# Kernel optimization log

Measured on AMD Instinct MI355X. Metric: run time of the kernel, lower is better.

The kernel has to match this reference:

```python
import jax, jax.numpy as jnp
import numpy as np

ALPHA, BETA, GAMMA = 0.05, 0.95, 0.95
GDEP = 2
HID = 64
IN_DIM = 3
OUT_DIM = 3
OUT_LEN = 12
PPH = 12.0  # points_per_hour
INV_SQRT2 = 0.7071067811865476


def _rownorm(a):
    # preprocessing(): add self-loop, row-normalize
    a = a + jnp.eye(a.shape[0], dtype=a.dtype)
    return a / jnp.sum(a, axis=-1, keepdims=True)


def _gcrn(x, A, P, W, b):
    # DGCRN-style diffusion conv: h <- a*x + b*A h + g*P h, concat hops, mlp
    h = x
    out = [x]
    for _ in range(GDEP):
        h = (ALPHA * x
             + BETA * jnp.einsum('bvc,vw->bwc', h, A)
             + GAMMA * jnp.einsum('bvc,vw->bwc', h, P))
        out.append(h)
    return jnp.concatenate(out, -1) @ W + b


def _cell_step(xin, H, A1, A1T, P, W, b):
    # one GRU-style step; W/b stacked as [gz1, gz2, gr1, gr2, gc1, gc2]
    comb = jnp.concatenate([xin, H], -1)
    z = jax.nn.sigmoid(_gcrn(comb, A1, P, W[0], b[0]) + _gcrn(comb, A1T, P, W[1], b[1]))
    r = jax.nn.sigmoid(_gcrn(comb, A1, P, W[2], b[2]) + _gcrn(comb, A1T, P, W[3], b[3]))
    temp = jnp.concatenate([xin, r * H], -1)
    C = jnp.tanh(_gcrn(temp, A1, P, W[4], b[4]) + _gcrn(temp, A1T, P, W[5], b[5]))
    H = z * H + (1.0 - z) * C
    return H, C


def _encode(xs, H0, C0, A1, A1T, P, W, b):
    def body(carry, xin):
        H, C = _cell_step(xin, carry[0], A1, A1T, P, W, b)
        return (H, C), None
    (H, C), _ = jax.lax.scan(body, (H0, C0), xs)
    return H, C


def _forward(x, seqs_time, adj, predefined_A, H1_0, C1_0, H2_0, C2_0,
             W_encD, b_encD, W_encAD, b_encAD, W_dec, b_dec, W_fc, b_fc,
             W_aggH, b_aggH, W_aggC, b_aggC, W_camH, b_camH, W_camC, b_camC,
             wL, bL, wH, bH):
    B, Cin, N, T = x.shape
    A1 = _rownorm(adj)
    A1T = _rownorm(adj.T)
    P = predefined_A
    # level-1 db1 (Haar) wavelet along time
    xe, xo = x[..., 0::2], x[..., 1::2]
    xAD = (xe + xo) * INV_SQRT2  # approximation coeffs (B,C,N,T/2)
    xD = (xe - xo) * INV_SQRT2   # detail coeffs
    # downsampled time-of-day index feature
    hour = (seqs_time[:, -2, :] + 0.5) * 23.0
    minute = (seqs_time[:, -1, :] + 0.5) * 59.0
    hidx = jnp.floor((hour * 60.0 + minute) / (60.0 / PPH))  # (B,T)
    t_ds = hidx[:, ::2]                                      # (B,T/2)
    Th = xD.shape[-1]
    tfeat = jnp.broadcast_to(t_ds.T[:, :, None, None], (Th, B, N, 1)).astype(x.dtype)
    xsD = jnp.concatenate([jnp.transpose(xD, (3, 0, 2, 1)), tfeat], -1)   # (Th,B,N,in+1)
    xsAD = jnp.concatenate([jnp.transpose(xAD, (3, 0, 2, 1)), tfeat], -1)
    H1, C1 = _encode(xsD, H1_0, C1_0, A1, A1T, P, W_encD, b_encD)
    H2, C2 = _encode(xsAD, H2_0, C2_0, A1, A1T, P, W_encAD, b_encAD)
    # learnable IDWT fusion + interleave (even cols = L, odd cols = H)
    def fuse(a, b2):
        L = (a * wL + bL) + (b2 * wL + bL)
        Hh = (a * wH + bH) + (b2 * wH + bH)
        return jnp.stack([L, Hh], -1).reshape(B, N, 2 * HID)
    Hm, Cm = fuse(H1, H2), fuse(C1, C2)
    # out_dim=3 <= 6 -> 0.3*cam + 0.7*agg branch
    H = 0.3 * (Hm @ W_camH + b_camH) + 0.7 * (jnp.concatenate([H1, H2], -1) @ W_aggH + b_aggH)
    C = 0.3 * (Cm @ W_camC + b_camC) + 0.7 * (jnp.concatenate([C1, C2], -1) @ W_aggC + b_aggC)
    # decoder (eval path, no curriculum sampling)
    tod = jnp.floor((seqs_time[:, 2, :] + 0.5) * 6.0)  # (B,T)
    todf = jnp.broadcast_to(tod.T[:OUT_LEN, :, None, None], (OUT_LEN, B, N, 1)).astype(x.dtype)
    def dec_body(carry, t):
        Hc, Cc, din = carry
        xin = jnp.concatenate([din, t], -1)  # (B,N,out_dim+1)
        Hc, Cc = _cell_step(xin, Hc, A1, A1T, P, W_dec, b_dec)
        out = Hc @ W_fc + b_fc               # (B,N,out_dim)
        return (Hc, Cc, out), out
    _, ys = jax.lax.scan(dec_body, (H, C, jnp.zeros((B, N, OUT_DIM), x.dtype)), todf)
    # replicate torch stack(dim=1).view(B,N,out_dim,out_len).permute(0,2,1,3)
    flat = jnp.transpose(ys, (1, 2, 0, 3)).reshape(B, N, OUT_DIM, OUT_LEN)
    return jnp.transpose(flat, (0, 2, 1, 3))


def setup_inputs() -> dict:
    key = jax.random.key(0)
    ks = jax.random.split(key, 24)
    B, N, T = 32, 325, 12
    d = {}
    d['x'] = jax.random.normal(ks[0], (B, IN_DIM, N, T), jnp.float32)
    d['seqs_time'] = jax.random.uniform(ks[1], (B, 4, T), jnp.float32) - 0.5
    d['adj'] = jax.random.uniform(ks[2], (N, N), jnp.float32)
    Pa = jax.random.uniform(ks[3], (N, N), jnp.float32)
    d['predefined_A'] = Pa / jnp.sum(Pa, -1, keepdims=True)
    for i, nm in enumerate(['H1_0', 'C1_0', 'H2_0', 'C2_0']):
        d[nm] = jax.random.normal(ks[4 + i], (B, N, HID), jnp.float32) * 0.1
    dim_in = (GDEP + 1) * (IN_DIM + HID + 1)  # 204
    for i, nm in enumerate(['W_encD', 'W_encAD', 'W_dec']):
        d[nm] = jax.random.normal(ks[8 + i], (6, dim_in, HID), jnp.float32) * 0.02
        d['b' + nm[1:]] = jnp.zeros((6, HID), jnp.float32)
    d['W_fc'] = jax.random.normal(ks[11], (HID, OUT_DIM), jnp.float32) * 0.02
    d['b_fc'] = jnp.zeros((OUT_DIM,), jnp.float32)
    for i, nm in enumerate(['aggH', 'aggC', 'camH', 'camC']):
        d['W_' + nm] = jax.random.normal(ks[12 + i], (2 * HID, HID), jnp.float32) * 0.02
        d['b_' + nm] = jnp.zeros((HID,), jnp.float32)
    d['wL'] = jax.random.normal(ks[16], (N, HID), jnp.float32) * 0.1
    d['bL'] = jnp.zeros((N, HID), jnp.float32)
    d['wH'] = jax.random.normal(ks[17], (N, HID), jnp.float32) * 0.1
    d['bH'] = jnp.zeros((N, HID), jnp.float32)
    return d


def reference(x, seqs_time, adj, predefined_A, H1_0, C1_0, H2_0, C2_0,
              W_encD, b_encD, W_encAD, b_encAD, W_dec, b_dec, W_fc, b_fc,
              W_aggH, b_aggH, W_aggC, b_aggC, W_camH, b_camH, W_camC, b_camC,
              wL, bL, wH, bH):
    return _forward(x, seqs_time, adj, predefined_A, H1_0, C1_0, H2_0, C2_0,
                    W_encD, b_encD, W_encAD, b_encAD, W_dec, b_dec, W_fc, b_fc,
                    W_aggH, b_aggH, W_aggC, b_aggC, W_camH, b_camH, W_camC, b_camC,
                    wL, bL, wH, bH)
```

## Files before the change

kernel.cpp:

```cpp
#include <hip/hip_runtime.h>
#include <math.h>

#define NN 325
#define BB 32
#define NB (NN*BB)
#define TENC 6
#define TDEC 12
#define WSET 65472
#define WT_SET (192*352)
#define M_SET (325*192)
#define G16_MAT (384*352)
#define PT_B 765952ull
#define PT_E 1531904ull
#define DP_B 3660800ull
#define DP_E 7321600ull

typedef _Float16 f16;
typedef f16 f16x4 __attribute__((ext_vector_type(4)));
typedef f16 f16x8 __attribute__((ext_vector_type(8)));
typedef float f32x4 __attribute__((ext_vector_type(4)));

static constexpr float ALPHA = 0.05f;
static constexpr float BETA  = 0.95f;
static constexpr float GAMMA = 0.95f;
static constexpr float ISQ2  = 0.7071067811865476f;

static constexpr size_t OFF_G    = 0;
static constexpr size_t OFF_RS   = OFF_G + 2ull*NN*NN;
static constexpr size_t OFF_RV   = OFF_RS + 650;
static constexpr size_t OFF_WEFF = OFF_RV + 1300;
static constexpr size_t OFF_WT   = OFF_WEFF + 3ull*WSET;
static constexpr size_t OFF_G16  = OFF_WT + (3ull*WT_SET)/2;
static constexpr size_t OFF_M    = OFF_G16 + (4ull*G16_MAT)/2;
static constexpr size_t OFF_WF   = OFF_M + 3ull*M_SET;
static constexpr size_t OFF_TV   = OFF_WF + 8192;
static constexpr size_t OFF_XS   = OFF_TV + 576;
static constexpr size_t OFF_PT   = OFF_XS + (2ull*TENC*NB*4)/2;
static constexpr size_t OFF_DP   = OFF_PT + (2ull*PT_E)/2;
static constexpr size_t OFF_ZR   = OFF_DP + (2ull*DP_E)/2;
static constexpr size_t OFF_HENC = OFF_ZR + 2ull*NB*64;
static constexpr size_t OFF_HDEC = OFF_HENC + 2ull*NB*64;

__device__ inline unsigned pk2(float a, float b) {
    union { f16 h[2]; unsigned u; } x;
    x.h[0] = (f16)a; x.h[1] = (f16)b; return x.u;
}
__device__ inline void st4h(f16* p, float a, float b, float c, float d) {
    f16x4 v; v[0]=(f16)a; v[1]=(f16)b; v[2]=(f16)c; v[3]=(f16)d;
    *(f16x4*)p = v;
}
__device__ inline f16x8 ld8_lds(const f16* p) {
    f16x4 lo = *(const f16x4*)p;
    f16x4 hi = *(const f16x4*)(p + 4);
    f16x8 r;
    r[0]=lo[0]; r[1]=lo[1]; r[2]=lo[2]; r[3]=lo[3];
    r[4]=hi[0]; r[5]=hi[1]; r[6]=hi[2]; r[7]=hi[3];
    return r;
}

__global__ void k_sums(const float* __restrict__ adj, float* rs, float* cs) {
    int v = blockIdx.x; int t = threadIdx.x;
    float sr = 0.f, sc = 0.f;
    for (int w = t; w < NN; w += 64) { sr += adj[v*NN + w]; sc += adj[w*NN + v]; }
    for (int o = 32; o > 0; o >>= 1) { sr += __shfl_down(sr, o); sc += __shfl_down(sc, o); }
    if (t == 0) { rs[v] = sr + 1.0f; cs[v] = sc + 1.0f; }
}

__global__ void k_buildG(const float* __restrict__ adj, const float* __restrict__ P,
                         const float* __restrict__ rs, const float* __restrict__ cs,
                         float* __restrict__ G) {
    int idx = blockIdx.x*256 + threadIdx.x;
    if (idx >= NN*NN) return;
    int w = idx / NN, v = idx % NN;
    float d = (v == w) ? 1.0f : 0.0f;
    float a1  = (adj[v*NN + w] + d) / rs[v];
    float a1t = (adj[w*NN + v] + d) / cs[v];
    float p = P[v*NN + w];
    G[idx]         = BETA*a1  + GAMMA*p;
    G[NN*NN + idx] = BETA*a1t + GAMMA*p;
}

__global__ __launch_bounds__(256) void k_gg(const float* __restrict__ G, float* __restrict__ G2) {
    int g = blockIdx.z;
    const float* A = G + (size_t)g*NN*NN;
    float* C = G2 + (size_t)g*NN*NN;
    int n0 = blockIdx.y*32, j0 = blockIdx.x*32;
    int tx = threadIdx.x & 31, ty = threadIdx.x >> 5;
    __shared__ float As[32][33];
    __shared__ float Bs[32][33];
    float acc[4] = {};
    for (int k0 = 0; k0 < NN; k0 += 32) {
        for (int l = threadIdx.x; l < 32*32; l += 256) {
            int i = l >> 5, kk = l & 31;
            int n = n0 + i, k = k0 + kk;
            As[i][kk] = (n < NN && k < NN) ? A[(size_t)n*NN + k] : 0.0f;
            int j = j0 + kk;
            Bs[i][kk] = (k0 + i < NN && j < NN) ? A[(size_t)(k0+i)*NN + j] : 0.0f;
        }
        __syncthreads();
        #pragma unroll 8
        for (int kk = 0; kk < 32; kk++) {
            float bv = Bs[kk][tx];
            #pragma unroll
            for (int i = 0; i < 4; i++) acc[i] = fmaf(As[ty + 8*i][kk], bv, acc[i]);
        }
        __syncthreads();
    }
    #pragma unroll
    for (int i = 0; i < 4; i++) {
        int n = n0 + ty + 8*i, j = j0 + tx;
        if (n < NN && j < NN) C[(size_t)n*NN + j] = acc[i];
    }
}

__global__ void k_g16(const float* __restrict__ G, const float* __restrict__ G2,
                      f16* __restrict__ G16) {
    int idx = blockIdx.x*256 + threadIdx.x;
    if (idx >= 4*G16_MAT) return;
    int m = idx / G16_MAT;
    int rem = idx - m*G16_MAT;
    int n = rem / 352, v = rem - n*352;
    int g = m >> 1, s = m & 1;
    float val = 0.0f;
    if (n < NN && v < NN) {
        float gv = G[(size_t)g*NN*NN + n*NN + v];
        float d = (n == v) ? ALPHA : 0.0f;
        val = (s == 0) ? (gv + d)
                       : (G2[(size_t)g*NN*NN + n*NN + v] + ALPHA*gv + d);
    }
    G16[idx] = (f16)val;
}

__global__ void k_rowsum(const float* __restrict__ G, const float* __restrict__ G2,
                         float* __restrict__ rv) {
    int row = blockIdx.x;
    int g = row / NN, n = row - g*NN;
    int t = threadIdx.x;
    float s1 = 0.f, s2 = 0.f;
    for (int v = t; v < NN; v += 64) {
        s1 += G[(size_t)g*NN*NN + n*NN + v];
        s2 += G2[(size_t)g*NN*NN + n*NN + v];
    }
    for (int o = 32; o > 0; o >>= 1) { s1 += __shfl_down(s1, o); s2 += __shfl_down(s2, o); }
    if (t == 0) {
        rv[(g*2 + 0)*NN + n] = ALPHA + s1;
        rv[(g*2 + 1)*NN + n] = ALPHA + ALPHA*s1 + s2;
    }
}

__global__ void k_weff3(const float* __restrict__ W0, const float* __restrict__ b0,
                        const float* __restrict__ W1, const float* __restrict__ b1,
                        const float* __restrict__ W2, const float* __restrict__ b2,
                        float* __restrict__ WeffAll) {
    int s = blockIdx.y;
    const float* W = (s == 0) ? W0 : (s == 1) ? W1 : W2;
    const float* b = (s == 0) ? b0 : (s == 1) ? b1 : b2;
    float* Wset = WeffAll + (size_t)s*WSET;
    float* Wzr = Wset;
    float* Wc  = Wset + 43520;
    float* bzr = Wset + 65280;
    float* bc  = Wset + 65408;
    int tid = blockIdx.x*256 + threadIdx.x;
    if (tid < 340*192) {
        int k = tid / 192, col = tid % 192;
        int g = col >> 6, oo = col & 63;
        const float* Wa = W + (2*g)*204*64;
        const float* Wb = W + (2*g+1)*204*64;
        float val;
        if (k < 68)       val = Wa[k*64+oo] + Wb[k*64+oo];
        else if (k < 204) val = Wa[k*64+oo];
        else              val = Wb[(k-136)*64+oo];
        if (g < 2) Wzr[k*128 + g*64 + oo] = val;
        else       Wc[k*64 + oo] = val;
    }
    if (blockIdx.x == 0 && threadIdx.x < 192) {
        int col = threadIdx.x, g = col >> 6, oo = col & 63;
        float bv = b[(2*g)*64+oo] + b[(2*g+1)*64+oo];
        if (g < 2) bzr[col] = bv; else bc[oo] = bv;
    }
}

__global__ void k_wt3(const float* __restrict__ WeffAll, f16* __restrict__ WtAll) {
    int s = blockIdx.y;
    const float* Weff = WeffAll + (size_t)s*WSET;
    f16* Wt = WtAll + (size_t)s*WT_SET;
    int idx = blockIdx.x*256 + threadIdx.x;
    if (idx >= 192*352) return;
    int o = idx / 352, k = idx - o*352;
    float v = 0.0f;
    if (k < 340) {
        int p = k / 68, c = k - p*68;
        if (c != 3) v = (o < 128) ? Weff[k*128 + o] : Weff[43520 + k*64 + (o - 128)];
    }
    Wt[idx] = (f16)v;
}

__global__ void k_M3(const float* __restrict__ WeffAll, const float* __restrict__ rv,
                     float* __restrict__ MAll) {
    int s = blockIdx.y;
    const float* Weff = WeffAll + (size_t)s*WSET;
    float* M = MAll + (size_t)s*M_SET;
    int idx = blockIdx.x*256 + threadIdx.x;
    if (idx >= 325*192) return;
    int n = idx / 192, q = idx - n*192;
    float acc;
    if (q < 128) {
        int o = q;
        acc = Weff[3*128 + o];
        #pragma unroll
        for (int p = 1; p <= 4; p++)
            acc += rv[(p-1)*NN + n] * Weff[(p*68 + 3)*128 + o];
        M[(size_t)n*128 + o] = acc;
    } else {
        int o = q - 128;
        acc = Weff[43520 + 3*64 + o];
        #pragma unroll
        for (int p = 1; p <= 4; p++)
            acc += rv[(p-1)*NN + n] * Weff[43520 + (p*68 + 3)*64 + o];
        M[325*128 + (size_t)n*64 + o] = acc;
    }
}

__global__ void k_wfuse(const float* __restrict__ Wcam, const float* __restrict__ Wagg,
                        f16* __restrict__ Wf) {
    int idx = blockIdx.x*256 + threadIdx.x;
    if (idx >= 64*256) return;
    int o = idx >> 8, k = idx & 255;
    float v = (k < 128) ? 0.3f*Wcam[(size_t)k*64 + o]
                        : 0.7f*Wagg[(size_t)(k-128)*64 + o];
    Wf[(size_t)o*256 + k] = (f16)v;
}

__global__ void k_tv(const float* __restrict__ st, float* __restrict__ tv) {
    int idx = blockIdx.x*256 + threadIdx.x;
    if (idx >= 18*32) return;
    int b = idx & 31, t = idx >> 5;
    float v;
    if (t < 6) {
        float hour   = (st[b*48 + 24 + 2*t] + 0.5f) * 23.0f;
        float minute = (st[b*48 + 36 + 2*t] + 0.5f) * 59.0f;
        v = floorf((hour*60.0f + minute) / 5.0f);
    } else {
        int td = t - 6;
        v = floorf((st[b*48 + 24 + td] + 0.5f) * 6.0f);
    }
    tv[idx] = v;
}

__global__ void k_xs16(const float* __restrict__ x, f16* __restrict__ xs) {
    int idx = blockIdx.x*256 + threadIdx.x;
    if (idx >= 2*TENC*NB*4) return;
    int c = idx & 3;
    int r = (idx >> 2) % NB;
    int t = (idx / (4*NB)) % TENC;
    int e = idx / (4*NB*TENC);
    int n = r / BB, b = r % BB;
    float val = 0.0f;
    if (c < 3) {
        float xe = x[((b*3 + c)*NN + n)*12 + 2*t];
        float xo = x[((b*3 + c)*NN + n)*12 + 2*t + 1];
        val = (e == 0) ? (xe - xo)*ISQ2 : (xe + xo)*ISQ2;
    }
    xs[idx] = (f16)val;
}

__global__ void k_initH(const float* __restrict__ H1_0, const float* __restrict__ H2_0,
                        float* __restrict__ Henc) {
    int idx = blockIdx.x*256 + threadIdx.x;
    if (idx >= 2*NB*64) return;
    int k = idx & 63;
    int r = (idx >> 6) % NB;
    int e = idx / (NB*64);
    int n = r / BB, b = r % BB;
    const float* src = e ? H2_0 : H1_0;
    Henc[idx] = src[((size_t)b*NN + n)*64 + k];
}

__global__ void k_initDP(const f16* __restrict__ xs, const float* __restrict__ H1_0,
                         const float* __restrict__ H2_0, f16* __restrict__ DP) {
    int idx = blockIdx.x*256 + threadIdx.x;
    if (idx >= 2*NB*92) return;
    int cc = idx % 92;
    int r = (idx / 92) % NB;
    int e = idx / (92*NB);
    int n = r >> 5, b = r & 31;
    f16* D0 = DP + (size_t)e*DP_E;
    if (cc < 68) {
        f16 v;
        if (cc < 3)       v = xs[(size_t)e*TENC*NB*4 + (size_t)r*4 + cc];
        else if (cc == 3) v = (f16)0.0f;
        else {
            const float* h0 = e ? H2_0 : H1_0;
            v = (f16)h0[((size_t)b*NN + n)*64 + (cc-4)];
        }
        D0[(size_t)r*352 + cc] = v;
    } else if (cc < 80) {
        D0[(size_t)r*352 + 340 + (cc-68)] = (f16)0.0f;
    } else {
        D0[DP_B + (size_t)r*352 + 340 + (cc-80)] = (f16)0.0f;
    }
}

__global__ void k_initPT(const f16* __restrict__ xs, const float* __restrict__ H1_0,
                         const float* __restrict__ H2_0, f16* __restrict__ PTb) {
    int idx = blockIdx.x*256 + threadIdx.x;
    if (idx >= 2*2176*352) return;
    int v = idx % 352;
    int j = (idx / 352) % 2176;
    int e = idx / (352*2176);
    f16* P0 = PTb + (size_t)e*PT_E;
    if (v >= NN) {
        P0[(size_t)j*352 + v] = (f16)0.0f;
        P0[PT_B + (size_t)j*352 + v] = (f16)0.0f;
        return;
    }
    int b = j / 68, c = j - b*68;
    f16 val;
    if (c < 3)       val = xs[(size_t)e*TENC*NB*4 + (size_t)(v*32+b)*4 + c];
    else if (c == 3) val = (f16)0.0f;
    else {
        const float* h0 = e ? H2_0 : H1_0;
        val = (f16)h0[((size_t)b*NN + v)*64 + (c-4)];
    }
    P0[(size_t)j*352 + v] = val;
}

struct KParams {
    const f16* G16;
    f16* PT;
    f16* DP;
    const f16* Wt;
    const float* Weff;
    const float* Mw;
    const float* tv;
    float* ZR;
    float* Henc;
    float* Hdec;
    const f16* xs;
    const float* wL; const float* bL; const float* wH; const float* bH;
    const float* bcam; const float* bagg;
    const f16* Wfuse;
    const float* Wfc; const float* bfc;
    float* out;
};

__device__ void phase_diff(const KParams& p, int par, int E) {
    int tid = threadIdx.x;
    int lane = tid & 63, w = tid >> 6;
    int wm = w >> 1, wn = w & 1;
    int l15 = lane & 15, lk = lane >> 4;
    int ntiles = 34*21*E;
    for (int idx = blockIdx.x; idx < ntiles; idx += gridDim.x) {
        int jt = idx % 34, rem = idx / 34;
        int Rt = rem % 21, e = rem / 21;
        const f16* X = p.PT + (size_t)e*PT_E + (size_t)par*PT_B;
        f16* D = p.DP + (size_t)e*DP_E + (size_t)par*DP_B;
        int j0 = jt*64, R0 = Rt*64;
        const f16* ap[2];
        #pragma unroll
        for (int a = 0; a < 2; a++)
            ap[a] = X + (size_t)(j0 + wm*32 + a*16 + l15)*352;
        const f16* bp[2]; int mv[2], nv[2];
        #pragma unroll
        for (int bt = 0; bt < 2; bt++) {
            int R = R0 + wn*32 + bt*16 + l15;
            int ok = (R < 1300);
            int Rc = ok ? R : 0;
            int m = Rc / 325, n = Rc - m*325;
            mv[bt] = ok ? m : -1; nv[bt] = n;
            bp[bt] = p.G16 + (size_t)m*G16_MAT + (size_t)n*352;
        }
        f32x4 acc[2][2] = {};
        #pragma unroll
        for (int k0 = 0; k0 < 352; k0 += 32) {
            f16x8 af[2], bf[2];
            #pragma unroll
            for (int a = 0; a < 2; a++) af[a] = *(const f16x8*)(ap[a] + k0 + lk*8);
            #pragma unroll
            for (int bt = 0; bt < 2; bt++) bf[bt] = *(const f16x8*)(bp[bt] + k0 + lk*8);
            #pragma unroll
            for (int a = 0; a < 2; a++)
                #pragma unroll
                for (int bt = 0; bt < 2; bt++)
                    acc[a][bt] = __builtin_amdgcn_mfma_f32_16x16x32_f16(af[a], bf[bt], acc[a][bt], 0,0,0);
        }
        #pragma unroll
        for (int bt = 0; bt < 2; bt++) {
            if (mv[bt] < 0) continue;
            int m = mv[bt], n = nv[bt];
            #pragma unroll
            for (int a = 0; a < 2; a++) {
                int jb = j0 + wm*32 + a*16 + lk*4;
                int b = jb / 68, c = jb - b*68;
                f16* dst = D + (size_t)(n*32 + b)*352 + (m+1)*68 + c;
                st4h(dst, acc[a][bt][0], acc[a][bt][1], acc[a][bt][2], acc[a][bt][3]);
            }
        }
    }
}

__device__ void phase_proj0(const KParams& p, int par, int E,
        const f16* WtB, int wt_str, const float* biasB, int bias_str,
        const float* MB, int m_str, const float* tvp, float* HstB) {
    int tid = threadIdx.x;
    int lane = tid & 63, w = tid >> 6;
    int wm = w >> 1, wn = w & 1;
    int l15 = lane & 15, lk = lane >> 4;
    int ntiles = 2*163*E;
    for (int idx = blockIdx.x; idx < ntiles; idx += gridDim.x) {
        int ob = idx & 1, rem = idx >> 1;
        int rt = rem % 163, e = rem / 163;
        const f16* Wt = WtB + (size_t)e*wt_str;
        const float* bias = biasB + (size_t)e*bias_str + 65280;
        const float* M = MB + (size_t)e*m_str;
        const f16* Dc = p.DP + (size_t)e*DP_E + (size_t)par*DP_B;
        f16* Dn = p.DP + (size_t)e*DP_E + (size_t)(par^1)*DP_B;
        f16* PTn = p.PT + (size_t)e*PT_E + (size_t)(par^1)*PT_B;
        float* ZR = p.ZR + (size_t)e*NB*64;
        float* Hs = HstB + (size_t)e*NB*64;
        int o0 = ob*64, r0 = rt*64;
        const f16* ap[2]; const f16* bp[2];
        #pragma unroll
        for (int a = 0; a < 2; a++) ap[a] = Wt + (size_t)(o0 + wm*32 + a*16 + l15)*352;
        #pragma unroll
        for (int bt = 0; bt < 2; bt++) bp[bt] = Dc + (size_t)(r0 + wn*32 + bt*16 + l15)*352;
        f32x4 acc[2][2] = {};
        #pragma unroll
        for (int k0 = 0; k0 < 352; k0 += 32) {
            f16x8 af[2], bf[2];
            #pragma unroll
            for (int a = 0; a < 2; a++) af[a] = *(const f16x8*)(ap[a] + k0 + lk*8);
            #pragma unroll
            for (int bt = 0; bt < 2; bt++) bf[bt] = *(const f16x8*)(bp[bt] + k0 + lk*8);
            #pragma unroll
            for (int a = 0; a < 2; a++)
                #pragma unroll
                for (int bt = 0; bt < 2; bt++)
                    acc[a][bt] = __builtin_amdgcn_mfma_f32_16x16x32_f16(af[a], bf[bt], acc[a][bt], 0,0,0);
        }
        #pragma unroll
        for (int bt = 0; bt < 2; bt++) {
            int r = r0 + wn*32 + bt*16 + l15;
            if (r < NB) {
                int n = r >> 5, b = r & 31;
                float tvb = tvp[b];
                #pragma unroll
                for (int a = 0; a < 2; a++) {
                    int oo = o0 + wm*32 + a*16 + lk*4;
                    float4 bs = *(const float4*)(bias + oo);
                    float4 ms = *(const float4*)(M + (size_t)n*128 + oo);
                    float p0 = acc[a][bt][0] + bs.x + tvb*ms.x;
                    float p1 = acc[a][bt][1] + bs.y + tvb*ms.y;
                    float p2 = acc[a][bt][2] + bs.z + tvb*ms.z;
                    float p3 = acc[a][bt][3] + bs.w + tvb*ms.w;
                    float s0 = 1.0f/(1.0f+expf(-p0)), s1 = 1.0f/(1.0f+expf(-p1));
                    float s2 = 1.0f/(1.0f+expf(-p2)), s3 = 1.0f/(1.0f+expf(-p3));
                    if (oo < 64) {
                        *(float4*)(ZR + (size_t)r*64 + oo) = make_float4(s0,s1,s2,s3);
                    } else {
                        int oh = oo - 64;
                        float4 h4 = *(const float4*)(Hs + (size_t)r*64 + oh);
                        float g0 = s0*h4.x, g1 = s1*h4.y, g2 = s2*h4.z, g3 = s3*h4.w;
                        st4h(Dn + (size_t)r*352 + 4 + oh, g0, g1, g2, g3);
                        size_t pb = (size_t)(b*68 + 4 + oh)*352 + n;
                        PTn[pb]       = (f16)g0;
                        PTn[pb + 352] = (f16)g1;
                        PTn[pb + 704] = (f16)g2;
                        PTn[pb + 1056]= (f16)g3;
                    }
                }
            }
        }
        if (ob == 0) {
            int row = tid >> 2, q = tid & 3;
            int r = r0 + row;
            if (r < NB) {
                f16 v = Dc[(size_t)r*352 + q];
                Dn[(size_t)r*352 + q] = v;
                PTn[(size_t)((r & 31)*68 + q)*352 + (r >> 5)] = v;
            }
        }
    }
}

__device__ void phase_proj1_enc(const KParams& p, int par, int t) {
    int tid = threadIdx.x;
    int lane = tid & 63, w = tid >> 6;
    int wm = w >> 1, wn = w & 1;
    int l15 = lane & 15, lk = lane >> 4;
    int ntiles = 163*2;
    for (int idx = blockIdx.x; idx < ntiles; idx += gridDim.x) {
        int rt = idx % 163, e = idx / 163;
        const f16* Wt = p.Wt + (size_t)e*WT_SET + 128*352;
        const float* bias = p.Weff + (size_t)e*WSET + 65408;
        const float* M = p.Mw + (size_t)e*M_SET + 325*128;
        const f16* Dc = p.DP + (size_t)e*DP_E + (size_t)par*DP_B;
        f16* Dn = p.DP + (size_t)e*DP_E + (size_t)(par^1)*DP_B;
        f16* PTn = p.PT + (size_t)e*PT_E + (size_t)(par^1)*PT_B;
        float* ZR = p.ZR + (size_t)e*NB*64;
        float* Hs = p.Henc + (size_t)e*NB*64;
        const float* tvv = p.tv + (size_t)t*32;
        int r0 = rt*64;
        const f16* ap[2]; const f16* bp[2];
        #pragma unroll
        for (int a = 0; a < 2; a++) ap[a] = Wt + (size_t)(wm*32 + a*16 + l15)*352;
        #pragma unroll
        for (int bt = 0; bt < 2; bt++) bp[bt] = Dc + (size_t)(r0 + wn*32 + bt*16 + l15)*352;
        f32x4 acc[2][2] = {};
        #pragma unroll
        for (int k0 = 0; k0 < 352; k0 += 32) {
            f16x8 af[2], bf[2];
            #pragma unroll
            for (int a = 0; a < 2; a++) af[a] = *(const f16x8*)(ap[a] + k0 + lk*8);
            #pragma unroll
            for (int bt = 0; bt < 2; bt++) bf[bt] = *(const f16x8*)(bp[bt] + k0 + lk*8);
            #pragma unroll
            for (int a = 0; a < 2; a++)
                #pragma unroll
                for (int bt = 0; bt < 2; bt++)
                    acc[a][bt] = __builtin_amdgcn_mfma_f32_16x16x32_f16(af[a], bf[bt], acc[a][bt], 0,0,0);
        }
        #pragma unroll
        for (int bt = 0; bt < 2; bt++) {
            int r = r0 + wn*32 + bt*16 + l15;
            if (r < NB) {
                int n = r >> 5, b = r & 31;
                float tvb = tvv[b];
                #pragma unroll
                for (int a = 0; a < 2; a++) {
                    int oo = wm*32 + a*16 + lk*4;
                    float4 bs = *(const float4*)(bias + oo);
                    float4 ms = *(const float4*)(M + (size_t)n*64 + oo);
                    float p0 = acc[a][bt][0] + bs.x + tvb*ms.x;
                    float p1 = acc[a][bt][1] + bs.y + tvb*ms.y;
                    float p2 = acc[a][bt][2] + bs.z + tvb*ms.z;
                    float p3 = acc[a][bt][3] + bs.w + tvb*ms.w;
                    float4 z4 = *(const float4*)(ZR + (size_t)r*64 + oo);
                    float4 h4 = *(const float4*)(Hs + (size_t)r*64 + oo);
                    float h0 = z4.x*h4.x + (1.0f - z4.x)*tanhf(p0);
                    float h1 = z4.y*h4.y + (1.0f - z4.y)*tanhf(p1);
                    float h2 = z4.z*h4.z + (1.0f - z4.z)*tanhf(p2);
                    float h3 = z4.w*h4.w + (1.0f - z4.w)*tanhf(p3);
                    *(float4*)(Hs + (size_t)r*64 + oo) = make_float4(h0,h1,h2,h3);
                    st4h(Dn + (size_t)r*352 + 4 + oo, h0, h1, h2, h3);
                    size_t pb = (size_t)(b*68 + 4 + oo)*352 + n;
                    PTn[pb]       = (f16)h0;
                    PTn[pb + 352] = (f16)h1;
                    PTn[pb + 704] = (f16)h2;
                    PTn[pb + 1056]= (f16)h3;
                }
            }
        }
        const f16* xn = nullptr;
        if (t < TENC-1) xn = p.xs + (size_t)(e*TENC + t + 1)*NB*4;
        if (xn) {
            int row = tid >> 2, q = tid & 3;
            int r = r0 + row;
            if (r < NB) {
                f16 v = (q < 3) ? xn[(size_t)r*4 + q] : (f16)0.0f;
                Dn[(size_t)r*352 + q] = v;
                PTn[(size_t)((r & 31)*68 + q)*352 + (r >> 5)] = v;
            }
        }
    }
}

__device__ void phase_proj1_dec(const KParams& p, int par, int t, f16* smem) {
    int tid = threadIdx.x;
    int lane = tid & 63, w = tid >> 6;
    int wm = w >> 1, wn = w & 1;
    int l15 = lane & 15, lk = lane >> 4;
    const f16* Wt = p.Wt + 2*WT_SET + 128*352;
    const float* bias = p.Weff + 2*WSET + 65408;
    const float* M = p.Mw + 2*M_SET + 325*128;
    const f16* Dc = p.DP + (size_t)par*DP_B;
    f16* Dn = p.DP + (size_t)(par^1)*DP_B;
    f16* PTn = p.PT + (size_t)(par^1)*PT_B;
    const float* tvv = p.tv + (size_t)(6 + t)*32;
    for (int idx = blockIdx.x; idx < 163; idx += gridDim.x) {
        int r0 = idx*64;
        const f16* ap[2]; const f16* bp[2];
        #pragma unroll
        for (int a = 0; a < 2; a++) ap[a] = Wt + (size_t)(wm*32 + a*16 + l15)*352;
        #pragma unroll
        for (int bt = 0; bt < 2; bt++) bp[bt] = Dc + (size_t)(r0 + wn*32 + bt*16 + l15)*352;
        f32x4 acc[2][2] = {};
        #pragma unroll
        for (int k0 = 0; k0 < 352; k0 += 32) {
            f16x8 af[2], bf[2];
            #pragma unroll
            for (int a = 0; a < 2; a++) af[a] = *(const f16x8*)(ap[a] + k0 + lk*8);
            #pragma unroll
            for (int bt = 0; bt < 2; bt++) bf[bt] = *(const f16x8*)(bp[bt] + k0 + lk*8);
            #pragma unroll
            for (int a = 0; a < 2; a++)
                #pragma unroll
                for (int bt = 0; bt < 2; bt++)
                    acc[a][bt] = __builtin_amdgcn_mfma_f32_16x16x32_f16(af[a], bf[bt], acc[a][bt], 0,0,0);
        }
        #pragma unroll
        for (int bt = 0; bt < 2; bt++) {
            int r = r0 + wn*32 + bt*16 + l15;
            int rl = wn*32 + bt*16 + l15;
            if (r < NB) {
                int n = r >> 5, b = r & 31;
                float tvb = tvv[b];
                #pragma unroll
                for (int a = 0; a < 2; a++) {
                    int oo = wm*32 + a*16 + lk*4;
                    float4 bs = *(const float4*)(bias + oo);
                    float4 ms = *(const float4*)(M + (size_t)n*64 + oo);
                    float p0 = acc[a][bt][0] + bs.x + tvb*ms.x;
                    float p1 = acc[a][bt][1] + bs.y + tvb*ms.y;
                    float p2 = acc[a][bt][2] + bs.z + tvb*ms.z;
                    float p3 = acc[a][bt][3] + bs.w + tvb*ms.w;
                    float4 z4 = *(const float4*)(p.ZR + (size_t)r*64 + oo);
                    float4 h4 = *(const float4*)(p.Hdec + (size_t)r*64 + oo);
                    float h0 = z4.x*h4.x + (1.0f - z4.x)*tanhf(p0);
                    float h1 = z4.y*h4.y + (1.0f - z4.y)*tanhf(p1);
                    float h2 = z4.z*h4.z + (1.0f - z4.z)*tanhf(p2);
                    float h3 = z4.w*h4.w + (1.0f - z4.w)*tanhf(p3);
                    *(float4*)(p.Hdec + (size_t)r*64 + oo) = make_float4(h0,h1,h2,h3);
                    st4h(Dn + (size_t)r*352 + 4 + oo, h0, h1, h2, h3);
                    size_t pb = (size_t)(b*68 + 4 + oo)*352 + n;
                    PTn[pb]       = (f16)h0;
                    PTn[pb + 352] = (f16)h1;
                    PTn[pb + 704] = (f16)h2;
                    PTn[pb + 1056]= (f16)h3;
                    st4h(smem + rl*68 + oo, h0, h1, h2, h3);
                }
            }
        }
        __syncthreads();
        for (int q = tid; q < 192; q += 256) {
            int row = q / 3, c = q - row*3;
            int r = r0 + row;
            if (r < NB) {
                float a = p.bfc[c];
                #pragma unroll 8
                for (int k = 0; k < 64; k++)
                    a = fmaf((float)smem[row*68 + k], p.Wfc[k*3 + c], a);
                int n = r >> 5, b = r & 31;
                int qq = t*3 + c;
                int oq = qq / 12, lq = qq - oq*12;
                p.out[(((size_t)b*3 + oq)*NN + n)*12 + lq] = a;
                if (t < TDEC-1) {
                    Dn[(size_t)r*352 + c] = (f16)a;
                    PTn[(size_t)((r & 31)*68 + c)*352 + (r >> 5)] = (f16)a;
                }
            }
        }
        if (t < TDEC-1 && tid < 64) {
            int r = r0 + tid;
            if (r < NB) {
                Dn[(size_t)r*352 + 3] = (f16)0.0f;
                PTn[(size_t)((r & 31)*68 + 3)*352 + (r >> 5)] = (f16)0.0f;
            }
        }
        __syncthreads();
    }
}

__device__ void phase_fuse(const KParams& p, f16* smem) {
    int tid = threadIdx.x;
    int lane = tid & 63, wave = tid >> 6;
    int wm = wave >> 1, wn = wave & 1;
    int l15 = lane & 15, lk = lane >> 4;
    const float* H1 = p.Henc;
    const float* H2 = p.Henc + (size_t)NB*64;
    unsigned* La = (unsigned*)smem;
    f16* Dn = p.DP;
    f16* PTn = p.PT;
    for (int idx = blockIdx.x; idx < 163; idx += gridDim.x) {
        int r0 = idx*64;
        for (int l = tid; l < 64*64; l += 256) {
            int i = l >> 6, k = l & 63;
            int r = r0 + i;
            unsigned val = 0;
            if (r < NB) {
                int n = r >> 5;
                float h1 = H1[(size_t)r*64 + k], h2 = H2[(size_t)r*64 + k];
                float s = h1 + h2;
                val = pk2(s*p.wL[n*64+k] + 2.0f*p.bL[n*64+k],
                          s*p.wH[n*64+k] + 2.0f*p.bH[n*64+k]);
            }
            La[i*132 + k] = val;
        }
        for (int l = tid; l < 64*32; l += 256) {
            int i = l >> 5, kp = l & 31;
            int r = r0 + i;
            unsigned v1 = 0, v2 = 0;
            if (r < NB) {
                float2 a = *(const float2*)(H1 + (size_t)r*64 + 2*kp);
                float2 b = *(const float2*)(H2 + (size_t)r*64 + 2*kp);
                v1 = pk2(a.x, a.y);
                v2 = pk2(b.x, b.y);
            }
            La[i*132 + 64 + kp] = v1;
            La[i*132 + 96 + kp] = v2;
        }
        __syncthreads();
        f32x4 acc[2][2] = {};
        for (int k0 = 0; k0 < 256; k0 += 32) {
            f16x8 afr[2], bfr[2];
            #pragma unroll
            for (int a = 0; a < 2; a++)
                afr[a] = ld8_lds(smem + (wm*32 + a*16 + l15)*264 + k0 + lk*8);
            #pragma unroll
            for (int b = 0; b < 2; b++)
                bfr[b] = *(const f16x8*)(p.Wfuse + (size_t)(wn*32 + b*16 + l15)*256 + k0 + lk*8);
            #pragma unroll
            for (int a = 0; a < 2; a++)
                #pragma unroll
                for (int b = 0; b < 2; b++)
                    acc[a][b] = __builtin_amdgcn_mfma_f32_16x16x32_f16(afr[a], bfr[b], acc[a][b], 0,0,0);
        }
        #pragma unroll
        for (int a = 0; a < 2; a++) {
            #pragma unroll
            for (int b = 0; b < 2; b++) {
                int o = wn*32 + b*16 + l15;
                float bo = 0.3f*p.bcam[o] + 0.7f*p.bagg[o];
                #pragma unroll
                for (int rr = 0; rr < 4; rr++) {
                    int r = r0 + wm*32 + a*16 + lk*4 + rr;
                    if (r >= NB) continue;
                    float val = acc[a][b][rr] + bo;
                    p.Hdec[(size_t)r*64 + o] = val;
                    Dn[(size_t)r*352 + 4 + o] = (f16)val;
                    PTn[(size_t)((r & 31)*68 + 4 + o)*352 + (r >> 5)] = (f16)val;
                }
            }
        }
        {
            int r = r0 + (tid >> 2), q = tid & 3;
            if (r < NB) {
                Dn[(size_t)r*352 + q] = (f16)0.0f;
                PTn[(size_t)((r & 31)*68 + q)*352 + (r >> 5)] = (f16)0.0f;
            }
        }
        __syncthreads();
    }
}

__global__ __launch_bounds__(256) void g_diff(KParams p, int par, int E) { phase_diff(p, par, E); }
__global__ __launch_bounds__(256) void g_proj0e(KParams p, int par, int t) {
    phase_proj0(p, par, 2, p.Wt, WT_SET, p.Weff, WSET, p.Mw, M_SET,
                p.tv + (size_t)t*32, p.Henc);
}
__global__ __launch_bounds__(256) void g_proj0d(KParams p, int par, int t) {
    phase_proj0(p, par, 1, p.Wt + 2*WT_SET, 0, p.Weff + 2*WSET, 0,
                p.Mw + 2*M_SET, 0, p.tv + (size_t)(6 + t)*32, p.Hdec);
}
__global__ __launch_bounds__(256) void g_proj1e(KParams p, int par, int t) { phase_proj1_enc(p, par, t); }
__global__ __launch_bounds__(256) void g_proj1d(KParams p, int par, int t) {
    __shared__ f16 smem[64*68];
    phase_proj1_dec(p, par, t, smem);
}
__global__ __launch_bounds__(256) void g_fuse(KParams p) {
    __shared__ f16 smem[64*264];
    phase_fuse(p, smem);
}

extern "C" void kernel_launch(void* const* d_in, const int* in_sizes, int n_in,
                              void* d_out, int out_size, void* d_ws, size_t ws_size,
                              hipStream_t stream) {
    const float* x      = (const float*)d_in[0];
    const float* st     = (const float*)d_in[1];
    const float* adj    = (const float*)d_in[2];
    const float* P      = (const float*)d_in[3];
    const float* H1_0   = (const float*)d_in[4];
    const float* H2_0   = (const float*)d_in[6];
    const float* W_encD = (const float*)d_in[8];
    const float* b_encD = (const float*)d_in[9];
    const float* W_encAD= (const float*)d_in[10];
    const float* b_encAD= (const float*)d_in[11];
    const float* W_dec  = (const float*)d_in[12];
    const float* b_dec  = (const float*)d_in[13];
    const float* W_fc   = (const float*)d_in[14];
    const float* b_fc   = (const float*)d_in[15];
    const float* W_aggH = (const float*)d_in[16];
    const float* b_aggH = (const float*)d_in[17];
    const float* W_camH = (const float*)d_in[20];
    const float* b_camH = (const float*)d_in[21];
    const float* wL     = (const float*)d_in[24];
    const float* bL     = (const float*)d_in[25];
    const float* wH     = (const float*)d_in[26];
    const float* bH     = (const float*)d_in[27];

    float* ws   = (float*)d_ws;
    float* G    = ws + OFF_G;
    float* rs   = ws + OFF_RS;
    float* cs   = rs + NN;
    float* rv   = ws + OFF_RV;
    float* Weff = ws + OFF_WEFF;
    f16*   Wt   = (f16*)(ws + OFF_WT);
    f16*   G16  = (f16*)(ws + OFF_G16);
    float* Mw   = ws + OFF_M;
    f16*   Wf   = (f16*)(ws + OFF_WF);
    float* tv   = ws + OFF_TV;
    f16*   xs   = (f16*)(ws + OFF_XS);
    f16*   PT   = (f16*)(ws + OFF_PT);
    f16*   DP   = (f16*)(ws + OFF_DP);
    float* ZR   = ws + OFF_ZR;
    float* G2   = ZR;
    float* Henc = ws + OFF_HENC;
    float* Hdec = ws + OFF_HDEC;

    k_sums<<<NN, 64, 0, stream>>>(adj, rs, cs);
    k_buildG<<<(NN*NN + 255)/256, 256, 0, stream>>>(adj, P, rs, cs, G);
    k_gg<<<dim3(11,11,2), 256, 0, stream>>>(G, G2);
    k_g16<<<(4*G16_MAT + 255)/256, 256, 0, stream>>>(G, G2, G16);
    k_rowsum<<<650, 64, 0, stream>>>(G, G2, rv);
    k_weff3<<<dim3(255,3), 256, 0, stream>>>(W_encD, b_encD, W_encAD, b_encAD,
                                             W_dec, b_dec, Weff);
    k_wt3<<<dim3((192*352 + 255)/256, 3), 256, 0, stream>>>(Weff, Wt);
    k_M3<<<dim3((325*192 + 255)/256, 3), 256, 0, stream>>>(Weff, rv, Mw);
    k_wfuse<<<64, 256, 0, stream>>>(W_camH, W_aggH, Wf);
    k_tv<<<3, 256, 0, stream>>>(st, tv);
    k_xs16<<<(2*TENC*NB*4 + 255)/256, 256, 0, stream>>>(x, xs);
    k_initH<<<(2*NB*64 + 255)/256, 256, 0, stream>>>(H1_0, H2_0, Henc);
    k_initDP<<<(2*NB*92 + 255)/256, 256, 0, stream>>>(xs, H1_0, H2_0, DP);
    k_initPT<<<(2*2176*352 + 255)/256, 256, 0, stream>>>(xs, H1_0, H2_0, PT);

    KParams prm;
    prm.G16 = G16; prm.PT = PT; prm.DP = DP;
    prm.Wt = Wt; prm.Weff = Weff; prm.Mw = Mw; prm.tv = tv;
    prm.ZR = ZR; prm.Henc = Henc; prm.Hdec = Hdec;
    prm.xs = xs;
    prm.wL = wL; prm.bL = bL; prm.wH = wH; prm.bH = bH;
    prm.bcam = b_camH; prm.bagg = b_aggH; prm.Wfuse = Wf;
    prm.Wfc = W_fc; prm.bfc = b_fc;
    prm.out = (float*)d_out;

    int par = 0;
    for (int t = 0; t < TENC; t++) {
        g_diff<<<1428, 256, 0, stream>>>(prm, par, 2);
        g_proj0e<<<652, 256, 0, stream>>>(prm, par, t);
        par ^= 1;
        g_diff<<<1428, 256, 0, stream>>>(prm, par, 2);
        g_proj1e<<<326, 256, 0, stream>>>(prm, par, t);
        par ^= 1;
    }
    g_fuse<<<163, 256, 0, stream>>>(prm);
    for (int t = 0; t < TDEC; t++) {
        g_diff<<<714, 256, 0, stream>>>(prm, par, 1);
        g_proj0d<<<326, 256, 0, stream>>>(prm, par, t);
        par ^= 1;
        g_diff<<<714, 256, 0, stream>>>(prm, par, 1);
        g_proj1d<<<163, 256, 0, stream>>>(prm, par, t);
        par ^= 1;
    }
}
```

Before: 1.358 ms.

## Remap projection row tiles to node-major groups for coalesced transposed writes

Projection and fuse kernels now tile rows as 32 consecutive nodes times 2 batch columns, replacing 64 consecutive flattened rows. The transposed PT buffer is indexed by node along its contiguous dimension, so each tile's scattered f16 stores become runs of adjacent nodes. The cost is extra padded tiles (176 instead of 163, with idle lanes in the last node group) and strided reads of the D rows. The fuse kernel also swaps MFMA operand roles so its outputs can be written as float4 and 4-wide f16 stores.

```diff
diff --git a/kernel.cpp b/kernel.cpp
--- a/kernel.cpp
+++ b/kernel.cpp
@@ -14,6 +14,7 @@
 #define PT_E 1531904ull
 #define DP_B 3660800ull
 #define DP_E 7321600ull
+#define NGB 176
 
 typedef _Float16 f16;
 typedef f16 f16x4 __attribute__((ext_vector_type(4)));
@@ -406,10 +407,11 @@
     int lane = tid & 63, w = tid >> 6;
     int wm = w >> 1, wn = w & 1;
     int l15 = lane & 15, lk = lane >> 4;
-    int ntiles = 2*163*E;
+    int ntiles = 2*NGB*E;
     for (int idx = blockIdx.x; idx < ntiles; idx += gridDim.x) {
         int ob = idx & 1, rem = idx >> 1;
-        int rt = rem % 163, e = rem / 163;
+        int rt = rem % NGB, e = rem / NGB;
+        int ng = rt >> 4, bpx = rt & 15;
         const f16* Wt = WtB + (size_t)e*wt_str;
         const float* bias = biasB + (size_t)e*bias_str + 65280;
         const float* M = MB + (size_t)e*m_str;
@@ -418,12 +420,18 @@
         f16* PTn = p.PT + (size_t)e*PT_E + (size_t)(par^1)*PT_B;
         float* ZR = p.ZR + (size_t)e*NB*64;
         float* Hs = HstB + (size_t)e*NB*64;
-        int o0 = ob*64, r0 = rt*64;
-        const f16* ap[2]; const f16* bp[2];
+        int o0 = ob*64;
+        int bcol = bpx*2 + wn;
+        const f16* ap[2]; const f16* bfp[2];
         #pragma unroll
         for (int a = 0; a < 2; a++) ap[a] = Wt + (size_t)(o0 + wm*32 + a*16 + l15)*352;
         #pragma unroll
-        for (int bt = 0; bt < 2; bt++) bp[bt] = Dc + (size_t)(r0 + wn*32 + bt*16 + l15)*352;
+        for (int bt = 0; bt < 2; bt++) {
+            int n = ng*32 + bt*16 + l15;
+            int r = n*32 + bcol;
+            int rc = (n < NN) ? r : 0;
+            bfp[bt] = Dc + (size_t)rc*352;
+        }
         f32x4 acc[2][2] = {};
         #pragma unroll
         for (int k0 = 0; k0 < 352; k0 += 32) {
@@ -431,7 +439,7 @@
             #pragma unroll
             for (int a = 0; a < 2; a++) af[a] = *(const f16x8*)(ap[a] + k0 + lk*8);
             #pragma unroll
-            for (int bt = 0; bt < 2; bt++) bf[bt] = *(const f16x8*)(bp[bt] + k0 + lk*8);
+            for (int bt = 0; bt < 2; bt++) bf[bt] = *(const f16x8*)(bfp[bt] + k0 + lk*8);
             #pragma unroll
             for (int a = 0; a < 2; a++)
                 #pragma unroll
@@ -440,9 +448,10 @@
         }
         #pragma unroll
         for (int bt = 0; bt < 2; bt++) {
-            int r = r0 + wn*32 + bt*16 + l15;
-            if (r < NB) {
-                int n = r >> 5, b = r & 31;
+            int n = ng*32 + bt*16 + l15;
+            if (n < NN) {
+                int b = bcol;
+                int r = n*32 + b;
                 float tvb = tvp[b];
                 #pragma unroll
                 for (int a = 0; a < 2; a++) {
@@ -472,12 +481,14 @@
             }
         }
         if (ob == 0) {
-            int row = tid >> 2, q = tid & 3;
-            int r = r0 + row;
-            if (r < NB) {
+            int n_l = tid & 31, b_l = (tid >> 5) & 1, q = tid >> 6;
+            int n = ng*32 + n_l;
+            if (n < NN) {
+                int b = bpx*2 + b_l;
+                int r = n*32 + b;
                 f16 v = Dc[(size_t)r*352 + q];
                 Dn[(size_t)r*352 + q] = v;
-                PTn[(size_t)((r & 31)*68 + q)*352 + (r >> 5)] = v;
+                PTn[(size_t)(b*68 + q)*352 + n] = v;
             }
         }
     }
@@ -488,9 +499,10 @@
     int lane = tid & 63, w = tid >> 6;
     int wm = w >> 1, wn = w & 1;
     int l15 = lane & 15, lk = lane >> 4;
-    int ntiles = 163*2;
+    int ntiles = NGB*2;
     for (int idx = blockIdx.x; idx < ntiles; idx += gridDim.x) {
-        int rt = idx % 163, e = idx / 163;
+        int rt = idx % NGB, e = idx / NGB;
+        int ng = rt >> 4, bpx = rt & 15;
         const f16* Wt = p.Wt + (size_t)e*WT_SET + 128*352;
         const float* bias = p.Weff + (size_t)e*WSET + 65408;
         const float* M = p.Mw + (size_t)e*M_SET + 325*128;
@@ -500,12 +512,17 @@
         float* ZR = p.ZR + (size_t)e*NB*64;
         float* Hs = p.Henc + (size_t)e*NB*64;
         const float* tvv = p.tv + (size_t)t*32;
-        int r0 = rt*64;
-        const f16* ap[2]; const f16* bp[2];
+        int bcol = bpx*2 + wn;
+        const f16* ap[2]; const f16* bfp[2];
         #pragma unroll
         for (int a = 0; a < 2; a++) ap[a] = Wt + (size_t)(wm*32 + a*16 + l15)*352;
         #pragma unroll
-        for (int bt = 0; bt < 2; bt++) bp[bt] = Dc + (size_t)(r0 + wn*32 + bt*16 + l15)*352;
+        for (int bt = 0; bt < 2; bt++) {
+            int n = ng*32 + bt*16 + l15;
+            int r = n*32 + bcol;
+            int rc = (n < NN) ? r : 0;
+            bfp[bt] = Dc + (size_t)rc*352;
+        }
         f32x4 acc[2][2] = {};
         #pragma unroll
         for (int k0 = 0; k0 < 352; k0 += 32) {
@@ -513,7 +530,7 @@
             #pragma unroll
             for (int a = 0; a < 2; a++) af[a] = *(const f16x8*)(ap[a] + k0 + lk*8);
             #pragma unroll
-            for (int bt = 0; bt < 2; bt++) bf[bt] = *(const f16x8*)(bp[bt] + k0 + lk*8);
+            for (int bt = 0; bt < 2; bt++) bf[bt] = *(const f16x8*)(bfp[bt] + k0 + lk*8);
             #pragma unroll
             for (int a = 0; a < 2; a++)
                 #pragma unroll
@@ -522,9 +539,10 @@
         }
         #pragma unroll
         for (int bt = 0; bt < 2; bt++) {
-            int r = r0 + wn*32 + bt*16 + l15;
-            if (r < NB) {
-                int n = r >> 5, b = r & 31;
+            int n = ng*32 + bt*16 + l15;
+            if (n < NN) {
+                int b = bcol;
+                int r = n*32 + b;
                 float tvb = tvv[b];
                 #pragma unroll
                 for (int a = 0; a < 2; a++) {
@@ -554,12 +572,14 @@
         const f16* xn = nullptr;
         if (t < TENC-1) xn = p.xs + (size_t)(e*TENC + t + 1)*NB*4;
         if (xn) {
-            int row = tid >> 2, q = tid & 3;
-            int r = r0 + row;
-            if (r < NB) {
+            int n_l = tid & 31, b_l = (tid >> 5) & 1, q = tid >> 6;
+            int n = ng*32 + n_l;
+            if (n < NN) {
+                int b = bpx*2 + b_l;
+                int r = n*32 + b;
                 f16 v = (q < 3) ? xn[(size_t)r*4 + q] : (f16)0.0f;
                 Dn[(size_t)r*352 + q] = v;
-                PTn[(size_t)((r & 31)*68 + q)*352 + (r >> 5)] = v;
+                PTn[(size_t)(b*68 + q)*352 + n] = v;
             }
         }
     }
@@ -577,13 +597,19 @@
     f16* Dn = p.DP + (size_t)(par^1)*DP_B;
     f16* PTn = p.PT + (size_t)(par^1)*PT_B;
     const float* tvv = p.tv + (size_t)(6 + t)*32;
-    for (int idx = blockIdx.x; idx < 163; idx += gridDim.x) {
-        int r0 = idx*64;
-        const f16* ap[2]; const f16* bp[2];
+    for (int idx = blockIdx.x; idx < NGB; idx += gridDim.x) {
+        int ng = idx >> 4, bpx = idx & 15;
+        int bcol = bpx*2 + wn;
+        const f16* ap[2]; const f16* bfp[2];
         #pragma unroll
         for (int a = 0; a < 2; a++) ap[a] = Wt + (size_t)(wm*32 + a*16 + l15)*352;
         #pragma unroll
-        for (int bt = 0; bt < 2; bt++) bp[bt] = Dc + (size_t)(r0 + wn*32 + bt*16 + l15)*352;
+        for (int bt = 0; bt < 2; bt++) {
+            int n = ng*32 + bt*16 + l15;
+            int r = n*32 + bcol;
+            int rc = (n < NN) ? r : 0;
+            bfp[bt] = Dc + (size_t)rc*352;
+        }
         f32x4 acc[2][2] = {};
         #pragma unroll
         for (int k0 = 0; k0 < 352; k0 += 32) {
@@ -591,7 +617,7 @@
             #pragma unroll
             for (int a = 0; a < 2; a++) af[a] = *(const f16x8*)(ap[a] + k0 + lk*8);
             #pragma unroll
-            for (int bt = 0; bt < 2; bt++) bf[bt] = *(const f16x8*)(bp[bt] + k0 + lk*8);
+            for (int bt = 0; bt < 2; bt++) bf[bt] = *(const f16x8*)(bfp[bt] + k0 + lk*8);
             #pragma unroll
             for (int a = 0; a < 2; a++)
                 #pragma unroll
@@ -600,10 +626,11 @@
         }
         #pragma unroll
         for (int bt = 0; bt < 2; bt++) {
-            int r = r0 + wn*32 + bt*16 + l15;
-            int rl = wn*32 + bt*16 + l15;
-            if (r < NB) {
-                int n = r >> 5, b = r & 31;
+            int n = ng*32 + bt*16 + l15;
+            int sl = wn*32 + bt*16 + l15;
+            if (n < NN) {
+                int b = bcol;
+                int r = n*32 + b;
                 float tvb = tvv[b];
                 #pragma unroll
                 for (int a = 0; a < 2; a++) {
@@ -627,34 +654,38 @@
                     PTn[pb + 352] = (f16)h1;
                     PTn[pb + 704] = (f16)h2;
                     PTn[pb + 1056]= (f16)h3;
-                    st4h(smem + rl*68 + oo, h0, h1, h2, h3);
+                    st4h(smem + sl*68 + oo, h0, h1, h2, h3);
                 }
             }
         }
         __syncthreads();
         for (int q = tid; q < 192; q += 256) {
-            int row = q / 3, c = q - row*3;
-            int r = r0 + row;
-            if (r < NB) {
+            int slot = q & 63, c = q >> 6;
+            int n = ng*32 + (slot & 31);
+            if (n < NN) {
+                int b = bpx*2 + (slot >> 5);
+                int r = n*32 + b;
                 float a = p.bfc[c];
                 #pragma unroll 8
                 for (int k = 0; k < 64; k++)
-                    a = fmaf((float)smem[row*68 + k], p.Wfc[k*3 + c], a);
-                int n = r >> 5, b = r & 31;
+                    a = fmaf((float)smem[slot*68 + k], p.Wfc[k*3 + c], a);
                 int qq = t*3 + c;
                 int oq = qq / 12, lq = qq - oq*12;
                 p.out[(((size_t)b*3 + oq)*NN + n)*12 + lq] = a;
                 if (t < TDEC-1) {
                     Dn[(size_t)r*352 + c] = (f16)a;
-                    PTn[(size_t)((r & 31)*68 + c)*352 + (r >> 5)] = (f16)a;
+                    PTn[(size_t)((size_t)(b*68 + c))*352 + n] = (f16)a;
                 }
             }
         }
         if (t < TDEC-1 && tid < 64) {
-            int r = r0 + tid;
-            if (r < NB) {
+            int slot = tid;
+            int n = ng*32 + (slot & 31);
+            if (n < NN) {
+                int b = bpx*2 + (slot >> 5);
+                int r = n*32 + b;
                 Dn[(size_t)r*352 + 3] = (f16)0.0f;
-                PTn[(size_t)((r & 31)*68 + 3)*352 + (r >> 5)] = (f16)0.0f;
+                PTn[(size_t)(b*68 + 3)*352 + n] = (f16)0.0f;
             }
         }
         __syncthreads();
@@ -671,14 +702,15 @@
     unsigned* La = (unsigned*)smem;
     f16* Dn = p.DP;
     f16* PTn = p.PT;
-    for (int idx = blockIdx.x; idx < 163; idx += gridDim.x) {
-        int r0 = idx*64;
+    for (int idx = blockIdx.x; idx < NGB; idx += gridDim.x) {
+        int ng = idx >> 4, bpx = idx & 15;
         for (int l = tid; l < 64*64; l += 256) {
             int i = l >> 6, k = l & 63;
-            int r = r0 + i;
+            int n = ng*32 + (i & 31);
             unsigned val = 0;
-            if (r < NB) {
-                int n = r >> 5;
+            if (n < NN) {
+                int b = bpx*2 + (i >> 5);
+                int r = n*32 + b;
                 float h1 = H1[(size_t)r*64 + k], h2 = H2[(size_t)r*64 + k];
                 float s = h1 + h2;
                 val = pk2(s*p.wL[n*64+k] + 2.0f*p.bL[n*64+k],
@@ -688,13 +720,15 @@
         }
         for (int l = tid; l < 64*32; l += 256) {
             int i = l >> 5, kp = l & 31;
-            int r = r0 + i;
+            int n = ng*32 + (i & 31);
             unsigned v1 = 0, v2 = 0;
-            if (r < NB) {
+            if (n < NN) {
+                int b = bpx*2 + (i >> 5);
+                int r = n*32 + b;
                 float2 a = *(const float2*)(H1 + (size_t)r*64 + 2*kp);
-                float2 b = *(const float2*)(H2 + (size_t)r*64 + 2*kp);
+                float2 b2 = *(const float2*)(H2 + (size_t)r*64 + 2*kp);
                 v1 = pk2(a.x, a.y);
-                v2 = pk2(b.x, b.y);
+                v2 = pk2(b2.x, b2.y);
             }
             La[i*132 + 64 + kp] = v1;
             La[i*132 + 96 + kp] = v2;
@@ -705,38 +739,49 @@
             f16x8 afr[2], bfr[2];
             #pragma unroll
             for (int a = 0; a < 2; a++)
-                afr[a] = ld8_lds(smem + (wm*32 + a*16 + l15)*264 + k0 + lk*8);
-            #pragma unroll
-            for (int b = 0; b < 2; b++)
-                bfr[b] = *(const f16x8*)(p.Wfuse + (size_t)(wn*32 + b*16 + l15)*256 + k0 + lk*8);
+                afr[a] = *(const f16x8*)(p.Wfuse + (size_t)(wn*32 + a*16 + l15)*256 + k0 + lk*8);
+            #pragma unroll
+            for (int bt = 0; bt < 2; bt++)
+                bfr[bt] = ld8_lds(smem + (wm*32 + bt*16 + l15)*264 + k0 + lk*8);
             #pragma unroll
             for (int a = 0; a < 2; a++)
                 #pragma unroll
-                for (int b = 0; b < 2; b++)
-                    acc[a][b] = __builtin_amdgcn_mfma_f32_16x16x32_f16(afr[a], bfr[b], acc[a][b], 0,0,0);
-        }
-        #pragma unroll
-        for (int a = 0; a < 2; a++) {
-            #pragma unroll
-            for (int b = 0; b < 2; b++) {
-                int o = wn*32 + b*16 + l15;
-                float bo = 0.3f*p.bcam[o] + 0.7f*p.bagg[o];
+                for (int bt = 0; bt < 2; bt++)
+                    acc[a][bt] = __builtin_amdgcn_mfma_f32_16x16x32_f16(afr[a], bfr[bt], acc[a][bt], 0,0,0);
+        }
+        __syncthreads();
+        #pragma unroll
+        for (int bt = 0; bt < 2; bt++) {
+            int i = wm*32 + bt*16 + l15;
+            int n = ng*32 + (i & 31);
+            if (n < NN) {
+                int b = bpx*2 + (i >> 5);
+                int r = n*32 + b;
                 #pragma unroll
-                for (int rr = 0; rr < 4; rr++) {
-                    int r = r0 + wm*32 + a*16 + lk*4 + rr;
-                    if (r >= NB) continue;
-                    float val = acc[a][b][rr] + bo;
-                    p.Hdec[(size_t)r*64 + o] = val;
-                    Dn[(size_t)r*352 + 4 + o] = (f16)val;
-                    PTn[(size_t)((r & 31)*68 + 4 + o)*352 + (r >> 5)] = (f16)val;
+                for (int a = 0; a < 2; a++) {
+                    int ob = wn*32 + a*16 + lk*4;
+                    float v0 = acc[a][bt][0] + 0.3f*p.bcam[ob]   + 0.7f*p.bagg[ob];
+                    float v1 = acc[a][bt][1] + 0.3f*p.bcam[ob+1] + 0.7f*p.bagg[ob+1];
+                    float v2 = acc[a][bt][2] + 0.3f*p.bcam[ob+2] + 0.7f*p.bagg[ob+2];
+                    float v3 = acc[a][bt][3] + 0.3f*p.bcam[ob+3] + 0.7f*p.bagg[ob+3];
+                    *(float4*)(p.Hdec + (size_t)r*64 + ob) = make_float4(v0,v1,v2,v3);
+                    st4h(Dn + (size_t)r*352 + 4 + ob, v0, v1, v2, v3);
+                    size_t pb = (size_t)(b*68 + 4 + ob)*352 + n;
+                    PTn[pb]       = (f16)v0;
+                    PTn[pb + 352] = (f16)v1;
+                    PTn[pb + 704] = (f16)v2;
+                    PTn[pb + 1056]= (f16)v3;
                 }
             }
         }
         {
-            int r = r0 + (tid >> 2), q = tid & 3;
-            if (r < NB) {
+            int n_l = tid & 31, b_l = (tid >> 5) & 1, q = tid >> 6;
+            int n = ng*32 + n_l;
+            if (n < NN) {
+                int b = bpx*2 + b_l;
+                int r = n*32 + b;
                 Dn[(size_t)r*352 + q] = (f16)0.0f;
-                PTn[(size_t)((r & 31)*68 + q)*352 + (r >> 5)] = (f16)0.0f;
+                PTn[(size_t)(b*68 + q)*352 + n] = (f16)0.0f;
             }
         }
         __syncthreads();
@@ -836,19 +881,19 @@
     int par = 0;
     for (int t = 0; t < TENC; t++) {
         g_diff<<<1428, 256, 0, stream>>>(prm, par, 2);
-        g_proj0e<<<652, 256, 0, stream>>>(prm, par, t);
+        g_proj0e<<<2*NGB*2, 256, 0, stream>>>(prm, par, t);
         par ^= 1;
         g_diff<<<1428, 256, 0, stream>>>(prm, par, 2);
-        g_proj1e<<<326, 256, 0, stream>>>(prm, par, t);
+        g_proj1e<<<NGB*2, 256, 0, stream>>>(prm, par, t);
         par ^= 1;
     }
-    g_fuse<<<163, 256, 0, stream>>>(prm);
+    g_fuse<<<NGB, 256, 0, stream>>>(prm);
     for (int t = 0; t < TDEC; t++) {
         g_diff<<<714, 256, 0, stream>>>(prm, par, 1);
-        g_proj0d<<<326, 256, 0, stream>>>(prm, par, t);
+        g_proj0d<<<2*NGB, 256, 0, stream>>>(prm, par, t);
         par ^= 1;
         g_diff<<<714, 256, 0, stream>>>(prm, par, 1);
-        g_proj1d<<<163, 256, 0, stream>>>(prm, par, t);
+        g_proj1d<<<NGB, 256, 0, stream>>>(prm, par, t);
         par ^= 1;
     }
 }
```

After: 1.190 ms. 12.4% less time.
